# Optimization experiments

Measured on AMD Instinct MI355X. Metric: run time of the kernel, lower is better.

## Reference

```python
import jax, jax.numpy as jnp
import numpy as np

D_MODEL = 768
NUM_HEADS = 12
D_K = D_MODEL // NUM_HEADS


def setup_inputs() -> dict:
    key = jax.random.key(0)
    ks = jax.random.split(key, 9)
    B, N, C = 32, 577, D_MODEL
    s = 1.0 / np.sqrt(C)
    x = jax.random.normal(ks[0], (B, N, C), dtype=jnp.float32)
    Wq = jax.random.normal(ks[1], (C, C), dtype=jnp.float32) * s
    bq = jnp.zeros((C,), dtype=jnp.float32)
    Wk = jax.random.normal(ks[2], (C, C), dtype=jnp.float32) * s
    bk = jnp.zeros((C,), dtype=jnp.float32)
    Wv = jax.random.normal(ks[3], (C, C), dtype=jnp.float32) * s
    bv = jnp.zeros((C,), dtype=jnp.float32)
    Wo = jax.random.normal(ks[4], (C, C), dtype=jnp.float32) * s
    bo = jnp.zeros((C,), dtype=jnp.float32)
    return {"x": x, "Wq": Wq, "bq": bq, "Wk": Wk, "bk": bk,
            "Wv": Wv, "bv": bv, "Wo": Wo, "bo": bo}


def reference(x, Wq, bq, Wk, bk, Wv, bv, Wo, bo):
    B, N, C = x.shape
    H, dk = NUM_HEADS, D_K
    # Linear projections (torch Linear: x @ W.T + b)
    q = (x @ Wq.T + bq).reshape(B, N, H, dk).transpose(0, 2, 1, 3)  # [B,H,N,dk]
    k = (x @ Wk.T + bk).reshape(B, N, H, dk).transpose(0, 2, 1, 3)
    v = (x @ Wv.T + bv).reshape(B, N, H, dk).transpose(0, 2, 1, 3)
    scale = 1.0 / jnp.sqrt(jnp.asarray(dk, dtype=x.dtype))
    scores = jnp.einsum('bhnd,bhmd->bhnm', q, k) * scale  # [B,H,N,N]
    attn = jax.nn.softmax(scores, axis=-1)
    out = jnp.einsum('bhnm,bhmd->bhnd', attn, v)  # [B,H,N,dk]
    out = out.transpose(0, 2, 1, 3).reshape(B, N, C)
    return out @ Wo.T + bo
```

## Files before the change

kernel.cpp:

```cpp
#include <hip/hip_runtime.h>
#include <cstdint>
#include <cstddef>

typedef float  f32x4   __attribute__((ext_vector_type(4)));
typedef __bf16 bf16x8  __attribute__((ext_vector_type(8)));
typedef short  short8  __attribute__((ext_vector_type(8)));
typedef short  short4v __attribute__((ext_vector_type(4)));
typedef float  float4v __attribute__((ext_vector_type(4)));

#define DEVI __device__ __forceinline__

constexpr int Bb = 32, Nn = 577, Cc = 768, Hh = 12, DK = 64;
constexpr int Mm   = Bb * Nn;
constexpr int NQKV = 3 * Cc;
constexpr int NKPAD = 640;
constexpr int NT = 10;
#define QSCALE 0.1803368926f

DEVI short f2bf(float f) {
  __bf16 h = (__bf16)f;
  short s;
  __builtin_memcpy(&s, &h, 2);
  return s;
}

DEVI void gload16(const short* g, short* l) {
  __builtin_amdgcn_global_load_lds(
      (const __attribute__((address_space(1))) void*)g,
      (__attribute__((address_space(3))) void*)l, 16, 0, 0);
}

DEVI f32x4 mfma16(bf16x8 a, bf16x8 b, f32x4 c) {
  return __builtin_amdgcn_mfma_f32_16x16x32_bf16(a, b, c, 0, 0, 0);
}

DEVI bf16x8 frag(const short* lds, int rowbase, int kk, int lane) {
  int r = rowbase + (lane & 15);
  int g = ((kk << 2) + (lane >> 4)) ^ (r & 7);
  return *(const bf16x8*)(lds + r * 64 + g * 8);
}

DEVI void remap_grouped(int bid, int nbm, int nbn, int GM, int& bm, int& bn) {
  const int nwg = nbm * nbn;
  const int xcd = bid & 7, j = bid >> 3;
  const int q = nwg >> 3, r = nwg & 7;
  int wg = (xcd < r ? xcd * (q + 1) : r * (q + 1) + (xcd - r) * q) + j;
  const int per = GM * nbn;
  int grp = wg / per;
  int first = grp * GM;
  int sz = min(GM, nbm - first);
  int rem = wg - grp * per;
  bm = first + rem % sz;
  bn = rem / sz;
}


__global__ void k_cvt(const float* __restrict__ in, short* __restrict__ out, int n4) {
  int i = blockIdx.x * 256 + threadIdx.x;
  if (i >= n4) return;
  float4v v = *(const float4v*)(in + (size_t)i * 4);
  short4v o;
#pragma unroll
  for (int j = 0; j < 4; ++j) o[j] = f2bf(v[j]);
  *(short4v*)(out + (size_t)i * 4) = o;
}

__global__ void k_cvt_wqkv(const float* __restrict__ Wq, const float* __restrict__ Wk,
                           const float* __restrict__ Wv, short* __restrict__ out) {
  int i = blockIdx.x * 256 + threadIdx.x;
  int e = i * 4;
  if (e >= NQKV * Cc) return;
  const int WSZ = Cc * Cc;
  const float* src;
  if (e < WSZ)          src = Wq + e;
  else if (e < 2 * WSZ) src = Wk + (e - WSZ);
  else                  src = Wv + (e - 2 * WSZ);
  float4v v = *(const float4v*)src;
  short4v o;
#pragma unroll
  for (int j = 0; j < 4; ++j) o[j] = f2bf(v[j]);
  *(short4v*)(out + (size_t)e) = o;
}


DEVI void gemm_core(const short* __restrict__ A, const short* __restrict__ Bm,
                    int arows, int brows, int bm, int bn,
                    short* As0, short* Bs0, short* As1, short* Bs1,
                    f32x4 acc[4][4]) {
  const int tid = threadIdx.x;
  const int lane = tid & 63, w = tid >> 6, wm = w >> 1, wn = w & 1;
#pragma unroll
  for (int mi = 0; mi < 4; ++mi)
#pragma unroll
    for (int ni = 0; ni < 4; ++ni) acc[mi][ni] = (f32x4)0.0f;

  const int rr = tid >> 3, c = tid & 7;
  const int cs = (c ^ (rr & 7)) * 8;
  const short* pa[4];
  const short* pb[4];
#pragma unroll
  for (int i = 0; i < 4; ++i) {
    int r = rr + 32 * i;
    int ga = bm * 128 + r; if (ga > arows - 1) ga = arows - 1;
    int gb = bn * 128 + r; if (gb > brows - 1) gb = brows - 1;
    pa[i] = A  + (size_t)ga * Cc + cs;
    pb[i] = Bm + (size_t)gb * Cc + cs;
  }

  auto stage = [&](short* As, short* Bs) {
#pragma unroll
    for (int i = 0; i < 4; ++i) {
      gload16(pa[i], As + (i * 256 + w * 64) * 8);
      gload16(pb[i], Bs + (i * 256 + w * 64) * 8);
      pa[i] += 64; pb[i] += 64;
    }
  };
  auto compute = [&](const short* As, const short* Bs) {
#pragma unroll
    for (int kk = 0; kk < 2; ++kk) {
      bf16x8 af[4], bfr[4];
#pragma unroll
      for (int mi = 0; mi < 4; ++mi) af[mi]  = frag(As, wm * 64 + mi * 16, kk, lane);
#pragma unroll
      for (int ni = 0; ni < 4; ++ni) bfr[ni] = frag(Bs, wn * 64 + ni * 16, kk, lane);
#pragma unroll
      for (int mi = 0; mi < 4; ++mi)
#pragma unroll
        for (int ni = 0; ni < 4; ++ni)
          acc[mi][ni] = mfma16(af[mi], bfr[ni], acc[mi][ni]);
    }
  };

  stage(As0, Bs0);
  __syncthreads();
#pragma unroll 1
  for (int t2 = 0; t2 < 5; ++t2) {
    stage(As1, Bs1);
    compute(As0, Bs0);
    __syncthreads();
    stage(As0, Bs0);
    compute(As1, Bs1);
    __syncthreads();
  }
  stage(As1, Bs1);
  compute(As0, Bs0);
  __syncthreads();
  compute(As1, Bs1);
}

__global__ __launch_bounds__(256) void k_gemm_qkv(
    const short* __restrict__ A, const short* __restrict__ Bm,
    const float* __restrict__ bq, const float* __restrict__ bk, const float* __restrict__ bv,
    short* __restrict__ qv, short* __restrict__ kv, short* __restrict__ vv) {
  __shared__ short As0[128 * 64];
  __shared__ short Bs0[128 * 64];
  __shared__ short As1[128 * 64];
  __shared__ short Bs1[128 * 64];
  int bm, bn;
  remap_grouped((int)blockIdx.x, (Mm + 127) / 128, NQKV / 128, 2, bm, bn);
  f32x4 acc[4][4];
  gemm_core(A, Bm, Mm, NQKV, bm, bn, As0, Bs0, As1, Bs1, acc);

  const int lane = threadIdx.x & 63, w = threadIdx.x >> 6, wm = w >> 1, wn = w & 1;
  const int qi = lane & 15, gg = lane >> 4;
  const int cb = bn * 128 + wn * 64;
  const int proj = cb / Cc;
  const int within = cb - proj * Cc;
  const float* bias = proj == 0 ? bq : proj == 1 ? bk : bv;
  short* dst = proj == 0 ? qv : proj == 1 ? kv : vv;
  const float sc = proj == 0 ? QSCALE : 1.0f;
  const int hh = within >> 6;
  float bvv[4];
#pragma unroll
  for (int ni = 0; ni < 4; ++ni) bvv[ni] = bias[within + ni * 16 + qi];
#pragma unroll
  for (int mi = 0; mi < 4; ++mi)
#pragma unroll
    for (int r = 0; r < 4; ++r) {
      int row = bm * 128 + wm * 64 + mi * 16 + gg * 4 + r;
      if (row < Mm) {
        int b = row / Nn;
        int nn = row - b * Nn;
        size_t base = ((size_t)(b * Hh + hh) * Nn + nn) * DK;
#pragma unroll
        for (int ni = 0; ni < 4; ++ni)
          dst[base + ni * 16 + qi] = f2bf((acc[mi][ni][r] + bvv[ni]) * sc);
      }
    }
}

__global__ __launch_bounds__(256) void k_gemm_out(
    const short* __restrict__ A, const short* __restrict__ Bm,
    const float* __restrict__ bo, float* __restrict__ out) {
  __shared__ short As0[128 * 64];
  __shared__ short Bs0[128 * 64];
  __shared__ short As1[128 * 64];
  __shared__ short Bs1[128 * 64];
  int bm, bn;
  remap_grouped((int)blockIdx.x, (Mm + 127) / 128, Cc / 128, 8, bm, bn);
  f32x4 acc[4][4];
  gemm_core(A, Bm, Mm, Cc, bm, bn, As0, Bs0, As1, Bs1, acc);

  const int lane = threadIdx.x & 63, w = threadIdx.x >> 6, wm = w >> 1, wn = w & 1;
  const int cb = bn * 128 + wn * 64;
  float bvv[4];
#pragma unroll
  for (int ni = 0; ni < 4; ++ni) bvv[ni] = bo[cb + ni * 16 + (lane & 15)];
#pragma unroll
  for (int mi = 0; mi < 4; ++mi)
#pragma unroll
    for (int r = 0; r < 4; ++r) {
      int row = bm * 128 + wm * 64 + mi * 16 + ((lane >> 4) << 2) + r;
      if (row < Mm) {
#pragma unroll
        for (int ni = 0; ni < 4; ++ni)
          out[(size_t)row * Cc + cb + ni * 16 + (lane & 15)] = acc[mi][ni][r] + bvv[ni];
      }
    }
}

__global__ __launch_bounds__(256) void k_transpose_v(const short* __restrict__ v,
                                                     short* __restrict__ vt) {
  __shared__ short t[64 * 72];
  const int bid = blockIdx.x;
  const int ch = bid % NT, bh = bid / NT;
  const int tid = threadIdx.x;
  const short* vb = v + (size_t)bh * Nn * DK;
#pragma unroll
  for (int i = 0; i < 2; ++i) {
    int gi = i * 256 + tid;
    int r = gi >> 3, c = gi & 7;
    int n = ch * 64 + r;
    short8 val;
#pragma unroll
    for (int j = 0; j < 8; ++j) val[j] = 0;
    if (n < Nn) val = *(const short8*)(vb + (size_t)n * DK + c * 8);
    *(short8*)(t + r * 72 + c * 8) = val;
  }
  __syncthreads();
  short* ob = vt + (size_t)bh * DK * NKPAD + ch * 64;
#pragma unroll
  for (int i = 0; i < 2; ++i) {
    int gi = i * 256 + tid;
    int d = gi >> 3, cg = gi & 7;
    short8 o;
#pragma unroll
    for (int j = 0; j < 8; ++j) o[j] = t[(cg * 8 + j) * 72 + d];
    *(short8*)(ob + (size_t)d * NKPAD + cg * 8) = o;
  }
}

__global__ __launch_bounds__(256) void k_attn(const short* __restrict__ q,
                                              const short* __restrict__ k,
                                              const short* __restrict__ vt,
                                              short* __restrict__ ao) {
  __shared__ short Ks[2][64 * 64];
  __shared__ short Vs[2][64 * 64];
  __shared__ short Ps[4][16 * 64];
  int bid = (int)blockIdx.x;
  bid = (bid & 7) * 480 + (bid >> 3);
  const int qt = bid % NT, bh = bid / NT;
  const int bb = bh / Hh, hh = bh - bb * Hh;
  const int tid = threadIdx.x, lane = tid & 63, w = tid >> 6;
  const int qi = lane & 15, g = lane >> 4;

  const short* qb  = q  + (size_t)bh * Nn * DK;
  const short* kb  = k  + (size_t)bh * Nn * DK;
  const short* vtb = vt + (size_t)bh * DK * NKPAD;

  const int qrow = qt * 64 + w * 16 + qi;
  const bf16x8 qf0 = *(const bf16x8*)(qb + (size_t)qrow * DK + g * 8);
  const bf16x8 qf1 = *(const bf16x8*)(qb + (size_t)qrow * DK + 32 + g * 8);

  const int r0 = tid >> 3, cc = tid & 7;
  const int cs0 = (cc ^ (r0 & 7)) * 8;
  const short* kg = kb + r0 * DK + cs0;
  const short* vg = vtb + (size_t)r0 * NKPAD + cs0;
  short* const Kd0 = &Ks[0][w * 512]; short* const Kd1 = &Ks[1][w * 512];
  short* const Vd0 = &Vs[0][w * 512]; short* const Vd1 = &Vs[1][w * 512];

  auto stage = [&](short* Kd, short* Vd) {
    gload16(kg, Kd);          gload16(kg + 2048,  Kd + 2048);
    gload16(vg, Vd);          gload16(vg + 20480, Vd + 2048);
    kg += 4096;               vg += 64;
  };

  const int swq = qi & 7;
  const short* const KF00 = &Ks[0][qi * 64 + ((g    ) ^ swq) * 8];
  const short* const KF01 = &Ks[0][qi * 64 + ((g + 4) ^ swq) * 8];
  const short* const KF10 = &Ks[1][qi * 64 + ((g    ) ^ swq) * 8];
  const short* const KF11 = &Ks[1][qi * 64 + ((g + 4) ^ swq) * 8];
  const short* const VF00 = &Vs[0][qi * 64 + ((g    ) ^ swq) * 8];
  const short* const VF01 = &Vs[0][qi * 64 + ((g + 4) ^ swq) * 8];
  const short* const VF10 = &Vs[1][qi * 64 + ((g    ) ^ swq) * 8];
  const short* const VF11 = &Vs[1][qi * 64 + ((g + 4) ^ swq) * 8];
  short* const PW0 = &Ps[w][qi * 64 + (((0  + g) ^ (swq << 1)) << 2)];
  short* const PW1 = &Ps[w][qi * 64 + (((4  + g) ^ (swq << 1)) << 2)];
  short* const PW2 = &Ps[w][qi * 64 + (((8  + g) ^ (swq << 1)) << 2)];
  short* const PW3 = &Ps[w][qi * 64 + (((12 + g) ^ (swq << 1)) << 2)];
  const short* const PR0 = &Ps[w][qi * 64 + ((g    ) ^ swq) * 8];
  const short* const PR1 = &Ps[w][qi * 64 + ((g + 4) ^ swq) * 8];

  f32x4 accd[4];
#pragma unroll
  for (int nd = 0; nd < 4; ++nd) accd[nd] = (f32x4)0.0f;
  float ls = 0.f;

  auto compute = [&](const short* Kf0, const short* Kf1,
                     const short* Vf0, const short* Vf1, bool last) {
    f32x4 s[4];
#pragma unroll
    for (int ni = 0; ni < 4; ++ni) s[ni] = (f32x4)0.0f;
#pragma unroll
    for (int ni = 0; ni < 4; ++ni)
      s[ni] = mfma16(*(const bf16x8*)(Kf0 + ni * 1024), qf0, s[ni]);
#pragma unroll
    for (int ni = 0; ni < 4; ++ni)
      s[ni] = mfma16(*(const bf16x8*)(Kf1 + ni * 1024), qf1, s[ni]);
    if (last) {
#pragma unroll
      for (int ni = 0; ni < 4; ++ni)
#pragma unroll
        for (int r = 0; r < 4; ++r)
          if (ni || r) s[ni][r] = -1e30f;
      if (g) s[0][0] = -1e30f;
    }
    float rs = 0.f;
    short4v pk0, pk1, pk2, pk3;
#pragma unroll
    for (int r = 0; r < 4; ++r) { float p = exp2f(s[0][r]); rs += p; pk0[r] = f2bf(p); }
#pragma unroll
    for (int r = 0; r < 4; ++r) { float p = exp2f(s[1][r]); rs += p; pk1[r] = f2bf(p); }
#pragma unroll
    for (int r = 0; r < 4; ++r) { float p = exp2f(s[2][r]); rs += p; pk2[r] = f2bf(p); }
#pragma unroll
    for (int r = 0; r < 4; ++r) { float p = exp2f(s[3][r]); rs += p; pk3[r] = f2bf(p); }
    *(short4v*)PW0 = pk0; *(short4v*)PW1 = pk1;
    *(short4v*)PW2 = pk2; *(short4v*)PW3 = pk3;
    rs += __shfl_xor(rs, 16);
    rs += __shfl_xor(rs, 32);
    ls += rs;
    bf16x8 pa0 = *(const bf16x8*)PR0;
    bf16x8 pa1 = *(const bf16x8*)PR1;
#pragma unroll
    for (int nd = 0; nd < 4; ++nd)
      accd[nd] = mfma16(pa0, *(const bf16x8*)(Vf0 + nd * 1024), accd[nd]);
#pragma unroll
    for (int nd = 0; nd < 4; ++nd)
      accd[nd] = mfma16(pa1, *(const bf16x8*)(Vf1 + nd * 1024), accd[nd]);
  };

  stage(Kd0, Vd0);
  __syncthreads();
#pragma unroll 1
  for (int t2 = 0; t2 < 5; ++t2) {
    stage(Kd1, Vd1);
    compute(KF00, KF01, VF00, VF01, false);
    __syncthreads();
    if (t2 < 4) {
      stage(Kd0, Vd0);
      compute(KF10, KF11, VF10, VF11, false);
      __syncthreads();
    }
  }
  compute(KF10, KF11, VF10, VF11, true);

  float ls4[4];
#pragma unroll
  for (int r = 0; r < 4; ++r) ls4[r] = __shfl(ls, (g << 2) + r);
#pragma unroll
  for (int r = 0; r < 4; ++r) {
    int qr = qt * 64 + w * 16 + (g << 2) + r;
    if (qr < Nn) {
      float inv = 1.0f / ls4[r];
      size_t base = ((size_t)(bb * Nn + qr)) * Cc + hh * DK;
#pragma unroll
      for (int nd = 0; nd < 4; ++nd)
        ao[base + nd * 16 + qi] = f2bf(accd[nd][r] * inv);
    }
  }
}


extern "C" void kernel_launch(void* const* d_in, const int* in_sizes, int n_in,
                              void* d_out, int out_size, void* d_ws, size_t ws_size,
                              hipStream_t stream) {
  const float* x  = (const float*)d_in[0];
  const float* Wq = (const float*)d_in[1];
  const float* bq = (const float*)d_in[2];
  const float* Wk = (const float*)d_in[3];
  const float* bk = (const float*)d_in[4];
  const float* Wv = (const float*)d_in[5];
  const float* bv = (const float*)d_in[6];
  const float* Wo = (const float*)d_in[7];
  const float* bo = (const float*)d_in[8];
  float* out = (float*)d_out;

  char* ws = (char*)d_ws;
  size_t off = 0;
  auto alloc = [&](size_t bytes) {
    char* p = ws + off;
    off += (bytes + 255) & ~(size_t)255;
    return p;
  };
  short* xb   = (short*)alloc((size_t)Mm * Cc * 2);
  short* wqkv = (short*)alloc((size_t)NQKV * Cc * 2);
  short* wob  = (short*)alloc((size_t)Cc * Cc * 2);
  short* qb   = (short*)alloc((size_t)Bb * Hh * Nn * DK * 2);
  short* kb   = (short*)alloc((size_t)Bb * Hh * Nn * DK * 2);
  short* vb   = (short*)alloc((size_t)Bb * Hh * Nn * DK * 2);
  short* vtb  = (short*)alloc((size_t)Bb * Hh * DK * NKPAD * 2);
  short* aob  = xb;

  k_cvt<<<(Mm * Cc / 4 + 255) / 256, 256, 0, stream>>>(x, xb, Mm * Cc / 4);
  k_cvt_wqkv<<<(NQKV * Cc / 4 + 255) / 256, 256, 0, stream>>>(Wq, Wk, Wv, wqkv);
  k_cvt<<<(Cc * Cc / 4 + 255) / 256, 256, 0, stream>>>(Wo, wob, Cc * Cc / 4);

  const int nbm = (Mm + 127) / 128;
  k_gemm_qkv<<<nbm * (NQKV / 128), 256, 0, stream>>>(xb, wqkv, bq, bk, bv, qb, kb, vb);

  k_transpose_v<<<Bb * Hh * NT, 256, 0, stream>>>(vb, vtb);

  k_attn<<<Bb * Hh * NT, 256, 0, stream>>>(qb, kb, vtb, aob);

  k_gemm_out<<<nbm * (Cc / 128), 256, 0, stream>>>(aob, wob, bo, out);
}
```

Before: 225.9 us.

## Rewrite projection GEMMs with 256x256 tiles, 8 waves, 4-stage LDS pipeline

Measured after the change: 223.7 us. No clear change (-1.0%).

```diff
diff --git a/kernel.cpp b/kernel.cpp
--- a/kernel.cpp
+++ b/kernel.cpp
@@ -32,12 +32,6 @@
 
 DEVI f32x4 mfma16(bf16x8 a, bf16x8 b, f32x4 c) {
   return __builtin_amdgcn_mfma_f32_16x16x32_bf16(a, b, c, 0, 0, 0);
-}
-
-DEVI bf16x8 frag(const short* lds, int rowbase, int kk, int lane) {
-  int r = rowbase + (lane & 15);
-  int g = ((kk << 2) + (lane >> 4)) ^ (r & 7);
-  return *(const bf16x8*)(lds + r * 64 + g * 8);
 }
 
 DEVI void remap_grouped(int bid, int nbm, int nbn, int GM, int& bm, int& bn) {
@@ -83,87 +77,123 @@
 }
 
 
-DEVI void gemm_core(const short* __restrict__ A, const short* __restrict__ Bm,
-                    int arows, int brows, int bm, int bn,
-                    short* As0, short* Bs0, short* As1, short* Bs1,
-                    f32x4 acc[4][4]) {
+#define WAITV(N) asm volatile("s_waitcnt vmcnt(" #N ")" ::: "memory")
+
+#define PHASE(DKH, MH, STAGE_STMT, WAIT_STMT)                              \
+  {                                                                        \
+    const short* Ab_ = Al + (DKH) * 8192;                                  \
+    const short* Bb_ = Bl + (DKH) * 8192;                                  \
+    bf16x8 af_[4];                                                         \
+    _Pragma("unroll")                                                      \
+    for (int m_ = 0; m_ < 4; ++m_)                                         \
+      af_[m_] = *(const bf16x8*)(Ab_ + offA[(MH) * 4 + m_]);               \
+    if ((MH) == 0) {                                                       \
+      _Pragma("unroll")                                                    \
+      for (int n_ = 0; n_ < 4; ++n_)                                       \
+        bfr[n_] = *(const bf16x8*)(Bb_ + offB[n_]);                        \
+    }                                                                      \
+    STAGE_STMT;                                                            \
+    WAIT_STMT;                                                             \
+    __builtin_amdgcn_s_barrier();                                          \
+    __builtin_amdgcn_s_setprio(1);                                         \
+    _Pragma("unroll")                                                      \
+    for (int m_ = 0; m_ < 4; ++m_)                                         \
+      _Pragma("unroll")                                                    \
+      for (int n_ = 0; n_ < 4; ++n_)                                       \
+        acc[(MH) * 4 + m_][n_] = mfma16(af_[m_], bfr[n_], acc[(MH) * 4 + m_][n_]); \
+    __builtin_amdgcn_s_setprio(0);                                         \
+    __builtin_amdgcn_s_barrier();                                          \
+  }
+
+DEVI void gemm256_core(const short* __restrict__ A, const short* __restrict__ Bm,
+                       int arows, int bm, int bn,
+                       short* Al, short* Bl, f32x4 acc[8][4]) {
   const int tid = threadIdx.x;
-  const int lane = tid & 63, w = tid >> 6, wm = w >> 1, wn = w & 1;
-#pragma unroll
-  for (int mi = 0; mi < 4; ++mi)
-#pragma unroll
-    for (int ni = 0; ni < 4; ++ni) acc[mi][ni] = (f32x4)0.0f;
-
-  const int rr = tid >> 3, c = tid & 7;
-  const int cs = (c ^ (rr & 7)) * 8;
-  const short* pa[4];
-  const short* pb[4];
-#pragma unroll
-  for (int i = 0; i < 4; ++i) {
-    int r = rr + 32 * i;
-    int ga = bm * 128 + r; if (ga > arows - 1) ga = arows - 1;
-    int gb = bn * 128 + r; if (gb > brows - 1) gb = brows - 1;
-    pa[i] = A  + (size_t)ga * Cc + cs;
-    pb[i] = Bm + (size_t)gb * Cc + cs;
-  }
-
-  auto stage = [&](short* As, short* Bs) {
-#pragma unroll
-    for (int i = 0; i < 4; ++i) {
-      gload16(pa[i], As + (i * 256 + w * 64) * 8);
-      gload16(pb[i], Bs + (i * 256 + w * 64) * 8);
-      pa[i] += 64; pb[i] += 64;
-    }
+  const int lane = tid & 63, w = tid >> 6;
+  const int wm = w >> 2, wn = w & 3;
+  const int qi = lane & 15, g = lane >> 4;
+
+#pragma unroll
+  for (int m = 0; m < 8; ++m)
+#pragma unroll
+    for (int n = 0; n < 4; ++n) acc[m][n] = (f32x4)0.0f;
+
+  const int r0 = tid >> 2, gq = tid & 3;
+  const int gs0 = (gq ^ ((r0 + (r0 >> 2)) & 3)) * 8;
+  int ga0 = bm * 256 + r0;       if (ga0 > arows - 1) ga0 = arows - 1;
+  int ga1 = bm * 256 + 128 + r0; if (ga1 > arows - 1) ga1 = arows - 1;
+  const short* pA0 = A  + (size_t)ga0 * Cc + gs0;
+  const short* pA1 = A  + (size_t)ga1 * Cc + gs0;
+  const short* pB0 = Bm + (size_t)(bn * 256 + r0) * Cc + gs0;
+  const short* pB1 = Bm + (size_t)(bn * 256 + 128 + r0) * Cc + gs0;
+
+  auto stA = [&](int dkh, int coff) {
+    short* d = Al + dkh * 8192 + w * 512;
+    gload16(pA0 + coff, d);
+    gload16(pA1 + coff, d + 4096);
   };
-  auto compute = [&](const short* As, const short* Bs) {
-#pragma unroll
-    for (int kk = 0; kk < 2; ++kk) {
-      bf16x8 af[4], bfr[4];
-#pragma unroll
-      for (int mi = 0; mi < 4; ++mi) af[mi]  = frag(As, wm * 64 + mi * 16, kk, lane);
-#pragma unroll
-      for (int ni = 0; ni < 4; ++ni) bfr[ni] = frag(Bs, wn * 64 + ni * 16, kk, lane);
-#pragma unroll
-      for (int mi = 0; mi < 4; ++mi)
-#pragma unroll
-        for (int ni = 0; ni < 4; ++ni)
-          acc[mi][ni] = mfma16(af[mi], bfr[ni], acc[mi][ni]);
-    }
+  auto stB = [&](int dkh, int coff) {
+    short* d = Bl + dkh * 8192 + w * 512;
+    gload16(pB0 + coff, d);
+    gload16(pB1 + coff, d + 4096);
   };
 
-  stage(As0, Bs0);
-  __syncthreads();
+  int offA[8], offB[4];
+#pragma unroll
+  for (int m = 0; m < 8; ++m) {
+    int r = wm * 128 + m * 16 + qi;
+    offA[m] = r * 32 + ((g ^ ((r + (r >> 2)) & 3)) * 8);
+  }
+#pragma unroll
+  for (int n = 0; n < 4; ++n) {
+    int r = wn * 64 + n * 16 + qi;
+    offB[n] = r * 32 + ((g ^ ((r + (r >> 2)) & 3)) * 8);
+  }
+  bf16x8 bfr[4];
+
+  stA(0, 0);  stB(0, 0);
+  stA(1, 32); stB(1, 32);
+  stA(2, 64); stB(2, 64);
+  WAITV(4);
+  __builtin_amdgcn_s_barrier();
+
 #pragma unroll 1
-  for (int t2 = 0; t2 < 5; ++t2) {
-    stage(As1, Bs1);
-    compute(As0, Bs0);
-    __syncthreads();
-    stage(As0, Bs0);
-    compute(As1, Bs1);
-    __syncthreads();
-  }
-  stage(As1, Bs1);
-  compute(As0, Bs0);
-  __syncthreads();
-  compute(As1, Bs1);
-}
-
-__global__ __launch_bounds__(256) void k_gemm_qkv(
+  for (int i = 0; i < 5; ++i) {
+    const int ko = i * 128;
+    PHASE(0, 0, stA(3, ko + 96),  (void)0);
+    PHASE(0, 1, stB(3, ko + 96),  WAITV(8));
+    PHASE(1, 0, stA(0, ko + 128), (void)0);
+    PHASE(1, 1, stB(0, ko + 128), WAITV(8));
+    PHASE(2, 0, stA(1, ko + 160), (void)0);
+    PHASE(2, 1, stB(1, ko + 160), WAITV(8));
+    PHASE(3, 0, stA(2, ko + 192), (void)0);
+    PHASE(3, 1, stB(2, ko + 192), WAITV(8));
+  }
+  PHASE(0, 0, stA(3, 736), (void)0);
+  PHASE(0, 1, stB(3, 736), WAITV(8));
+  PHASE(1, 0, (void)0, (void)0);
+  PHASE(1, 1, (void)0, WAITV(4));
+  PHASE(2, 0, (void)0, (void)0);
+  PHASE(2, 1, (void)0, WAITV(0));
+  PHASE(3, 0, (void)0, (void)0);
+  PHASE(3, 1, (void)0, (void)0);
+}
+
+__global__ __launch_bounds__(512) void k_gemm_qkv(
     const short* __restrict__ A, const short* __restrict__ Bm,
     const float* __restrict__ bq, const float* __restrict__ bk, const float* __restrict__ bv,
     short* __restrict__ qv, short* __restrict__ kv, short* __restrict__ vv) {
-  __shared__ short As0[128 * 64];
-  __shared__ short Bs0[128 * 64];
-  __shared__ short As1[128 * 64];
-  __shared__ short Bs1[128 * 64];
+  __shared__ short Al[4 * 8192];
+  __shared__ short Bl[4 * 8192];
   int bm, bn;
-  remap_grouped((int)blockIdx.x, (Mm + 127) / 128, NQKV / 128, 2, bm, bn);
-  f32x4 acc[4][4];
-  gemm_core(A, Bm, Mm, NQKV, bm, bn, As0, Bs0, As1, Bs1, acc);
-
-  const int lane = threadIdx.x & 63, w = threadIdx.x >> 6, wm = w >> 1, wn = w & 1;
-  const int qi = lane & 15, gg = lane >> 4;
-  const int cb = bn * 128 + wn * 64;
+  remap_grouped((int)blockIdx.x, (Mm + 255) / 256, NQKV / 256, 4, bm, bn);
+  f32x4 acc[8][4];
+  gemm256_core(A, Bm, Mm, bm, bn, Al, Bl, acc);
+
+  const int lane = threadIdx.x & 63, w = threadIdx.x >> 6;
+  const int wm = w >> 2, wn = w & 3;
+  const int qi = lane & 15, g = lane >> 4;
+  const int cb = bn * 256 + wn * 64;
   const int proj = cb / Cc;
   const int within = cb - proj * Cc;
   const float* bias = proj == 0 ? bq : proj == 1 ? bk : bv;
@@ -172,49 +202,49 @@
   const int hh = within >> 6;
   float bvv[4];
 #pragma unroll
-  for (int ni = 0; ni < 4; ++ni) bvv[ni] = bias[within + ni * 16 + qi];
-#pragma unroll
-  for (int mi = 0; mi < 4; ++mi)
+  for (int n = 0; n < 4; ++n) bvv[n] = bias[within + n * 16 + qi];
+#pragma unroll
+  for (int m = 0; m < 8; ++m)
 #pragma unroll
     for (int r = 0; r < 4; ++r) {
-      int row = bm * 128 + wm * 64 + mi * 16 + gg * 4 + r;
+      int row = bm * 256 + wm * 128 + m * 16 + g * 4 + r;
       if (row < Mm) {
         int b = row / Nn;
         int nn = row - b * Nn;
         size_t base = ((size_t)(b * Hh + hh) * Nn + nn) * DK;
 #pragma unroll
-        for (int ni = 0; ni < 4; ++ni)
-          dst[base + ni * 16 + qi] = f2bf((acc[mi][ni][r] + bvv[ni]) * sc);
+        for (int n = 0; n < 4; ++n)
+          dst[base + n * 16 + qi] = f2bf((acc[m][n][r] + bvv[n]) * sc);
       }
     }
 }
 
-__global__ __launch_bounds__(256) void k_gemm_out(
+__global__ __launch_bounds__(512) void k_gemm_out(
     const short* __restrict__ A, const short* __restrict__ Bm,
     const float* __restrict__ bo, float* __restrict__ out) {
-  __shared__ short As0[128 * 64];
-  __shared__ short Bs0[128 * 64];
-  __shared__ short As1[128 * 64];
-  __shared__ short Bs1[128 * 64];
+  __shared__ short Al[4 * 8192];
+  __shared__ short Bl[4 * 8192];
   int bm, bn;
-  remap_grouped((int)blockIdx.x, (Mm + 127) / 128, Cc / 128, 8, bm, bn);
-  f32x4 acc[4][4];
-  gemm_core(A, Bm, Mm, Cc, bm, bn, As0, Bs0, As1, Bs1, acc);
-
-  const int lane = threadIdx.x & 63, w = threadIdx.x >> 6, wm = w >> 1, wn = w & 1;
-  const int cb = bn * 128 + wn * 64;
+  remap_grouped((int)blockIdx.x, (Mm + 255) / 256, Cc / 256, 8, bm, bn);
+  f32x4 acc[8][4];
+  gemm256_core(A, Bm, Mm, bm, bn, Al, Bl, acc);
+
+  const int lane = threadIdx.x & 63, w = threadIdx.x >> 6;
+  const int wm = w >> 2, wn = w & 3;
+  const int qi = lane & 15, g = lane >> 4;
+  const int cb = bn * 256 + wn * 64;
   float bvv[4];
 #pragma unroll
-  for (int ni = 0; ni < 4; ++ni) bvv[ni] = bo[cb + ni * 16 + (lane & 15)];
-#pragma unroll
-  for (int mi = 0; mi < 4; ++mi)
+  for (int n = 0; n < 4; ++n) bvv[n] = bo[cb + n * 16 + qi];
+#pragma unroll
+  for (int m = 0; m < 8; ++m)
 #pragma unroll
     for (int r = 0; r < 4; ++r) {
-      int row = bm * 128 + wm * 64 + mi * 16 + ((lane >> 4) << 2) + r;
+      int row = bm * 256 + wm * 128 + m * 16 + g * 4 + r;
       if (row < Mm) {
 #pragma unroll
-        for (int ni = 0; ni < 4; ++ni)
-          out[(size_t)row * Cc + cb + ni * 16 + (lane & 15)] = acc[mi][ni][r] + bvv[ni];
+        for (int n = 0; n < 4; ++n)
+          out[(size_t)row * Cc + cb + n * 16 + qi] = acc[m][n][r] + bvv[n];
       }
     }
 }
@@ -416,12 +446,12 @@
   k_cvt_wqkv<<<(NQKV * Cc / 4 + 255) / 256, 256, 0, stream>>>(Wq, Wk, Wv, wqkv);
   k_cvt<<<(Cc * Cc / 4 + 255) / 256, 256, 0, stream>>>(Wo, wob, Cc * Cc / 4);
 
-  const int nbm = (Mm + 127) / 128;
-  k_gemm_qkv<<<nbm * (NQKV / 128), 256, 0, stream>>>(xb, wqkv, bq, bk, bv, qb, kb, vb);
+  const int nbm = (Mm + 255) / 256;
+  k_gemm_qkv<<<nbm * (NQKV / 256), 512, 0, stream>>>(xb, wqkv, bq, bk, bv, qb, kb, vb);
 
   k_transpose_v<<<Bb * Hh * NT, 256, 0, stream>>>(vb, vtb);
 
   k_attn<<<Bb * Hh * NT, 256, 0, stream>>>(qb, kb, vtb, aob);
 
-  k_gemm_out<<<nbm * (Cc / 128), 256, 0, stream>>>(aob, wob, bo, out);
-}
+  k_gemm_out<<<nbm * (Cc / 256), 512, 0, stream>>>(aob, wob, bo, out);
+}
```
